# Kernel optimization log

Measured on AMD Instinct MI355X. Metric: run time of the kernel, lower is better.

The kernel has to match this reference:

```python
import jax, jax.numpy as jnp
import numpy as np

B, K, T, C = 4, 8, 2048, 64

def setup_inputs() -> dict:
    key = jax.random.key(0)
    ks = jax.random.split(key, 7)
    return {
        "x": jax.random.normal(ks[0], (B, K, T, C), dtype=jnp.float32),
        "Wq": jax.random.normal(ks[1], (C, C), dtype=jnp.float32) / np.sqrt(C),
        "bq": jax.random.normal(ks[2], (C,), dtype=jnp.float32) * 0.01,
        "Wk": jax.random.normal(ks[3], (C, C), dtype=jnp.float32) / np.sqrt(C),
        "bk": jax.random.normal(ks[4], (C,), dtype=jnp.float32) * 0.01,
        "Wv": jax.random.normal(ks[5], (C, C), dtype=jnp.float32) / np.sqrt(C),
        "bv": jax.random.normal(ks[6], (C,), dtype=jnp.float32) * 0.01,
    }

def reference(x, Wq, bq, Wk, bk, Wv, bv):
    c_dim = x.shape[-1]
    # torch nn.Linear: y = x @ W.T + b
    q = jnp.einsum('bktc,dc->bktd', x, Wq) + bq
    k = jnp.einsum('bktc,dc->bktd', x, Wk) + bk
    v = jnp.einsum('bktc,dc->bktd', x, Wv) + bv
    scores = jnp.einsum('bkic,bkjc->bkij', q, k) / jnp.sqrt(jnp.float32(c_dim))
    attn = jax.nn.softmax(scores, axis=-1)
    out = jnp.einsum('bkij,bkjc->bkic', attn, v)
    return out
```

## Files before the change

kernel.cpp:

```cpp
#include <hip/hip_runtime.h>


#define T_DIM 2048
#define NHEAD 32
#define HSTRIDE (T_DIM * 64)
#define QSCALE 0.18033688011112042f
#define SOFF  8.0f

#define SWZ(row, grp) ((row) * 64 + ((((grp) ^ ((row) & 7)) & 7) * 8))

typedef _Float16 h8 __attribute__((ext_vector_type(8)));
typedef _Float16 h4 __attribute__((ext_vector_type(4)));
typedef __fp16   g2 __attribute__((ext_vector_type(2)));
typedef float    f4 __attribute__((ext_vector_type(4)));

union H4U { h4 v; g2 p[2]; };
union H8U { h8 v; h4 h[2]; };

#if defined(__has_builtin)
#if __has_builtin(__builtin_amdgcn_exp2f)
#define EXP2(x) __builtin_amdgcn_exp2f(x)
#endif
#endif
#ifndef EXP2
__device__ inline float exp2_raw(float x) {
    float r;
    asm("v_exp_f32 %0, %1" : "=v"(r) : "v"(x));
    return r;
}
#define EXP2(x) exp2_raw(x)
#endif

__device__ inline h4 cvt4(f4 x) {
    H4U u;
    u.p[0] = __builtin_amdgcn_cvt_pkrtz(x[0], x[1]);
    u.p[1] = __builtin_amdgcn_cvt_pkrtz(x[2], x[3]);
    return u.v;
}

__global__ __launch_bounds__(256) void qkv_proj_kernel(
    const float* __restrict__ x,
    const float* __restrict__ Wq, const float* __restrict__ bq,
    const float* __restrict__ Wk, const float* __restrict__ bk,
    const float* __restrict__ Wv, const float* __restrict__ bv,
    _Float16* __restrict__ qh, _Float16* __restrict__ khT,
    _Float16* __restrict__ vtT)
{
    __shared__ _Float16 ws[3][64 * 64];
    __shared__ _Float16 xs[64 * 64];
    __shared__ float bsh[3][64];
    _Float16* ot = xs;

    const int tid  = threadIdx.x;
    const int row0 = blockIdx.x * 64;
    const int head = blockIdx.x >> 5;
    const int t0   = (blockIdx.x & 31) * 64;

    #pragma unroll
    for (int m = 0; m < 3; ++m) {
        const float* Wm = (m == 0) ? Wq : ((m == 1) ? Wk : Wv);
        const float* bm = (m == 0) ? bq : ((m == 1) ? bk : bv);
        #pragma unroll
        for (int pass = 0; pass < 4; ++pass) {
            const int idx = pass * 1024 + tid * 4;
            const int d = idx >> 6, c = idx & 63;
            f4 wv = *(const f4*)(Wm + idx);
            *(h4*)&ws[m][SWZ(d, c >> 3) + (c & 7)] = cvt4(wv);
        }
        if (tid < 64) bsh[m][tid] = bm[tid];
    }
    {
        const float* xb = x + (size_t)row0 * 64;
        #pragma unroll
        for (int pass = 0; pass < 4; ++pass) {
            const int idx = pass * 1024 + tid * 4;
            const int r = idx >> 6, c = idx & 63;
            f4 xv = *(const f4*)(xb + idx);
            *(h4*)&xs[SWZ(r, c >> 3) + (c & 7)] = cvt4(xv);
        }
    }
    __syncthreads();

    const int w    = tid >> 6;
    const int lane = tid & 63;
    const int l15  = lane & 15;
    const int qd   = lane >> 4;

    h8 af[2];
    #pragma unroll
    for (int ch = 0; ch < 2; ++ch)
        af[ch] = *(const h8*)&xs[SWZ(w * 16 + l15, ch * 4 + qd)];

    #pragma unroll
    for (int m = 0; m < 3; ++m) {
        h8 bf[4][2];
        #pragma unroll
        for (int ns = 0; ns < 4; ++ns)
            #pragma unroll
            for (int ch = 0; ch < 2; ++ch)
                bf[ns][ch] = *(const h8*)&ws[m][SWZ(ns * 16 + l15, ch * 4 + qd)];

        f4 acc[4];
        #pragma unroll
        for (int ns = 0; ns < 4; ++ns)
            acc[ns] = (f4){0.f, 0.f, 0.f, 0.f};
        #pragma unroll
        for (int ch = 0; ch < 2; ++ch)
            #pragma unroll
            for (int ns = 0; ns < 4; ++ns)
                acc[ns] = __builtin_amdgcn_mfma_f32_16x16x32_f16(
                    af[ch], bf[ns][ch], acc[ns], 0, 0, 0);

        __syncthreads();
        if (m < 2) {
            #pragma unroll
            for (int ns = 0; ns < 4; ++ns) {
                const int d = ns * 16 + l15;
                const float bias = bsh[m][d];
                #pragma unroll
                for (int r = 0; r < 4; ++r) {
                    const int t = w * 16 + qd * 4 + r;
                    float v = acc[ns][r] + bias;
                    if (m == 0) v *= QSCALE;
                    ot[SWZ(t, d >> 3) + (d & 7)] = (_Float16)v;
                }
            }
            __syncthreads();
            if (m == 0) {
                #pragma unroll
                for (int pass = 0; pass < 2; ++pass) {
                    const int t  = pass * 32 + (tid >> 3);
                    const int c0 = (tid & 7) * 8;
                    *(h8*)&qh[(size_t)(row0 + t) * 64 + c0] =
                        *(const h8*)&ot[SWZ(t, tid & 7)];
                }
            } else {
                #pragma unroll
                for (int pass = 0; pass < 2; ++pass) {
                    const int f    = pass * 2048 + tid * 8;
                    const int Jl   = f >> 10;
                    const int rest = f & 1023;
                    const int ch_  = rest >> 9;
                    const int qd_  = (rest >> 7) & 3;
                    const int l15_ = (rest >> 3) & 15;
                    h8 val = *(const h8*)&ot[SWZ(Jl * 16 + l15_, ch_ * 4 + qd_)];
                    *(h8*)&khT[(size_t)head * HSTRIDE + ((t0 >> 4) + Jl) * 1024 + rest] = val;
                }
            }
        } else {
            #pragma unroll
            for (int ns = 0; ns < 4; ++ns) {
                const int d = ns * 16 + l15;
                const float bias = bsh[2][d];
                const int tl = w * 16 + qd * 4;
                f4 pvf;
                #pragma unroll
                for (int r = 0; r < 4; ++r)
                    pvf[r] = acc[ns][r] + bias;
                *(h4*)&ot[SWZ(d, tl >> 3) + (tl & 7)] = cvt4(pvf);
            }
            __syncthreads();
            #pragma unroll
            for (int pass = 0; pass < 2; ++pass) {
                const int f   = pass * 2048 + tid * 8;
                const int qd3 = f >> 10;
                const int rem = f & 1023;
                const int c   = rem >> 4;
                const int g   = (rem & 15) >> 3;
                const int ta  = (2 * g) * 16 + qd3 * 4;
                const int tb  = ta + 16;
                H8U val;
                val.h[0] = *(const h4*)&ot[SWZ(c, ta >> 3) + (ta & 7)];
                val.h[1] = *(const h4*)&ot[SWZ(c, tb >> 3) + (tb & 7)];
                *(h8*)&vtT[(size_t)head * HSTRIDE + (t0 >> 6) * 4096 + f] = val.v;
            }
        }
    }
}

__global__ __launch_bounds__(256, 2) void attn_kernel(
    const _Float16* __restrict__ qh, const _Float16* __restrict__ khT,
    const _Float16* __restrict__ vtT, float* __restrict__ out)
{
    __shared__ float mrg[2][64][41];
    const int tid  = threadIdx.x;
    const int w    = tid >> 6;
    const int lane = tid & 63;
    const int l15  = lane & 15;
    const int qd   = lane >> 4;
    const int qgrp = w >> 1;
    const int kph  = w & 1;

    const int bid  = blockIdx.x;
    const int xcd  = bid & 7;
    const int slot = bid >> 3;
    const int head = xcd * 4 + (slot >> 5);
    const int q0   = (slot & 31) * 64 + qgrp * 32;

    h8 qf[2][2];
    #pragma unroll
    for (int is = 0; is < 2; ++is) {
        const _Float16* qp = qh + (size_t)(head * T_DIM + q0 + is * 16 + l15) * 64 + qd * 8;
        qf[is][0] = *(const h8*)qp;
        qf[is][1] = *(const h8*)(qp + 32);
    }

    const h4 vones = {(_Float16)1.0f, (_Float16)1.0f, (_Float16)1.0f, (_Float16)1.0f};
    f4 lacc[2] = {(f4){0.f,0.f,0.f,0.f}, (f4){0.f,0.f,0.f,0.f}};
    f4 oacc[2][4];
    #pragma unroll
    for (int is = 0; is < 2; ++is)
        #pragma unroll
        for (int cs = 0; cs < 4; ++cs)
            oacc[is][cs] = (f4){0.f, 0.f, 0.f, 0.f};

    const _Float16* kA = khT + (size_t)head * HSTRIDE + kph * 65536;
    const _Float16* kB = kA + 2048;
    const _Float16* vA = vtT + (size_t)head * HSTRIDE + kph * 65536;
    const int ko = lane * 8;
    const int vo = qd * 1024 + l15 * 16;

    h8 kf[4][2];
    #pragma unroll
    for (int jt = 0; jt < 4; ++jt)
        #pragma unroll
        for (int ch = 0; ch < 2; ++ch)
            kf[jt][ch] = *(const h8*)(((jt < 2) ? kA : kB) + (jt & 1) * 1024 + ch * 512 + ko);

    for (int kt = 0; kt < 16; ++kt) {
        H8U vf8[4][2];
        #pragma unroll
        for (int cs = 0; cs < 4; ++cs) {
            vf8[cs][0].v = *(const h8*)(vA + cs * 256 + vo);
            vf8[cs][1].v = *(const h8*)(vA + cs * 256 + vo + 8);
        }

        f4 st[4][2];
        #pragma unroll
        for (int jt = 0; jt < 4; ++jt)
            #pragma unroll
            for (int is = 0; is < 2; ++is)
                st[jt][is] = (f4){-SOFF, -SOFF, -SOFF, -SOFF};
        #pragma unroll
        for (int ch = 0; ch < 2; ++ch)
            #pragma unroll
            for (int jt = 0; jt < 4; ++jt)
                #pragma unroll
                for (int is = 0; is < 2; ++is)
                    st[jt][is] = __builtin_amdgcn_mfma_f32_16x16x32_f16(
                        kf[jt][ch], qf[is][ch], st[jt][is], 0, 0, 0);

        kA += 4096; kB += 4096;
        if (kt < 15) {
            #pragma unroll
            for (int jt = 0; jt < 4; ++jt)
                #pragma unroll
                for (int ch = 0; ch < 2; ++ch)
                    kf[jt][ch] = *(const h8*)(((jt < 2) ? kA : kB) + (jt & 1) * 1024 + ch * 512 + ko);
        }

        h4 pf[4][2];
        #pragma unroll
        for (int is = 0; is < 2; ++is)
            #pragma unroll
            for (int jt = 0; jt < 4; ++jt) {
                f4 p;
                p[0] = EXP2(st[jt][is][0]);
                p[1] = EXP2(st[jt][is][1]);
                p[2] = EXP2(st[jt][is][2]);
                p[3] = EXP2(st[jt][is][3]);
                pf[jt][is] = cvt4(p);
            }

        #pragma unroll
        for (int jt = 0; jt < 4; ++jt) {
            #pragma unroll
            for (int cs = 0; cs < 4; ++cs)
                #pragma unroll
                for (int is = 0; is < 2; ++is)
                    oacc[is][cs] = __builtin_amdgcn_mfma_f32_16x16x16f16(
                        pf[jt][is], vf8[cs][jt >> 1].h[jt & 1], oacc[is][cs], 0, 0, 0);
            #pragma unroll
            for (int is = 0; is < 2; ++is)
                lacc[is] = __builtin_amdgcn_mfma_f32_16x16x16f16(
                    pf[jt][is], vones, lacc[is], 0, 0, 0);
        }
        vA += 4096;
    }

    if (kph == 1) {
        #pragma unroll
        for (int is = 0; is < 2; ++is) {
            #pragma unroll
            for (int cs = 0; cs < 4; ++cs)
                #pragma unroll
                for (int r = 0; r < 4; ++r)
                    mrg[qgrp][lane][(is * 4 + cs) * 4 + r] = oacc[is][cs][r];
            #pragma unroll
            for (int r = 0; r < 4; ++r)
                mrg[qgrp][lane][32 + is * 4 + r] = lacc[is][r];
        }
    }
    __syncthreads();
    if (kph == 0) {
        #pragma unroll
        for (int is = 0; is < 2; ++is) {
            float linv[4];
            #pragma unroll
            for (int r = 0; r < 4; ++r)
                linv[r] = 1.f / (lacc[is][r] + mrg[qgrp][lane][32 + is * 4 + r]);
            #pragma unroll
            for (int cs = 0; cs < 4; ++cs) {
                const int c = cs * 16 + l15;
                #pragma unroll
                for (int r = 0; r < 4; ++r) {
                    const int t = q0 + is * 16 + qd * 4 + r;
                    float o = oacc[is][cs][r] + mrg[qgrp][lane][(is * 4 + cs) * 4 + r];
                    out[(size_t)(head * T_DIM + t) * 64 + c] = o * linv[r];
                }
            }
        }
    }
}

extern "C" void kernel_launch(void* const* d_in, const int* in_sizes, int n_in,
                              void* d_out, int out_size, void* d_ws, size_t ws_size,
                              hipStream_t stream)
{
    (void)in_sizes; (void)n_in; (void)out_size; (void)ws_size;
    const float* x  = (const float*)d_in[0];
    const float* Wq = (const float*)d_in[1];
    const float* bq = (const float*)d_in[2];
    const float* Wk = (const float*)d_in[3];
    const float* bk = (const float*)d_in[4];
    const float* Wv = (const float*)d_in[5];
    const float* bv = (const float*)d_in[6];
    float* out = (float*)d_out;

    _Float16* qh  = (_Float16*)d_ws;
    _Float16* khT = qh + (size_t)NHEAD * HSTRIDE;
    _Float16* vtT = khT + (size_t)NHEAD * HSTRIDE;

    hipLaunchKernelGGL(qkv_proj_kernel, dim3(1024), dim3(256), 0, stream,
                       x, Wq, bq, Wk, bk, Wv, bv, qh, khT, vtT);
    hipLaunchKernelGGL(attn_kernel, dim3(1024), dim3(256), 0, stream,
                       qh, khT, vtT, out);
}
```

Before: 131.0 us.

## Compute softmax row sums with VALU adds and shuffles instead of ones-MFMA

The attention kernel drops the extra MFMA against a ones matrix that accumulated the softmax denominators. It now adds the fp32 exp values per lane and reduces them across lanes with xor shuffles after the loop, then broadcasts the inverse with shuffles. The QKV projection also loads x straight from global memory into MFMA fragments, skipping the LDS staging buffer and one barrier. This trims matrix-core work in the inner loop and adds a few VALU adds and shuffles, and the row sum now uses unrounded fp32 probabilities.

Result: no change. 129.8 us (-0.9%).

```diff
diff --git a/kernel.cpp b/kernel.cpp
--- a/kernel.cpp
+++ b/kernel.cpp
@@ -38,6 +38,13 @@
     return u.v;
 }
 
+__device__ inline h8 cvt8(f4 a, f4 b) {
+    H8U r;
+    r.h[0] = cvt4(a);
+    r.h[1] = cvt4(b);
+    return r.v;
+}
+
 __global__ __launch_bounds__(256) void qkv_proj_kernel(
     const float* __restrict__ x,
     const float* __restrict__ Wq, const float* __restrict__ bq,
@@ -47,9 +54,8 @@
     _Float16* __restrict__ vtT)
 {
     __shared__ _Float16 ws[3][64 * 64];
-    __shared__ _Float16 xs[64 * 64];
+    __shared__ _Float16 ot[64 * 64];
     __shared__ float bsh[3][64];
-    _Float16* ot = xs;
 
     const int tid  = threadIdx.x;
     const int row0 = blockIdx.x * 64;
@@ -69,17 +75,6 @@
         }
         if (tid < 64) bsh[m][tid] = bm[tid];
     }
-    {
-        const float* xb = x + (size_t)row0 * 64;
-        #pragma unroll
-        for (int pass = 0; pass < 4; ++pass) {
-            const int idx = pass * 1024 + tid * 4;
-            const int r = idx >> 6, c = idx & 63;
-            f4 xv = *(const f4*)(xb + idx);
-            *(h4*)&xs[SWZ(r, c >> 3) + (c & 7)] = cvt4(xv);
-        }
-    }
-    __syncthreads();
 
     const int w    = tid >> 6;
     const int lane = tid & 63;
@@ -87,9 +82,16 @@
     const int qd   = lane >> 4;
 
     h8 af[2];
-    #pragma unroll
-    for (int ch = 0; ch < 2; ++ch)
-        af[ch] = *(const h8*)&xs[SWZ(w * 16 + l15, ch * 4 + qd)];
+    {
+        const float* xp = x + (size_t)(row0 + w * 16 + l15) * 64 + qd * 8;
+        #pragma unroll
+        for (int ch = 0; ch < 2; ++ch) {
+            f4 a0 = *(const f4*)(xp + ch * 32);
+            f4 a1 = *(const f4*)(xp + ch * 32 + 4);
+            af[ch] = cvt8(a0, a1);
+        }
+    }
+    __syncthreads();
 
     #pragma unroll
     for (int m = 0; m < 3; ++m) {
@@ -182,7 +184,7 @@
     const _Float16* __restrict__ qh, const _Float16* __restrict__ khT,
     const _Float16* __restrict__ vtT, float* __restrict__ out)
 {
-    __shared__ float mrg[2][64][41];
+    __shared__ float mrg[2][64][35];
     const int tid  = threadIdx.x;
     const int w    = tid >> 6;
     const int lane = tid & 63;
@@ -205,8 +207,7 @@
         qf[is][1] = *(const h8*)(qp + 32);
     }
 
-    const h4 vones = {(_Float16)1.0f, (_Float16)1.0f, (_Float16)1.0f, (_Float16)1.0f};
-    f4 lacc[2] = {(f4){0.f,0.f,0.f,0.f}, (f4){0.f,0.f,0.f,0.f}};
+    f4 rs4[2] = {(f4){0.f,0.f,0.f,0.f}, (f4){0.f,0.f,0.f,0.f}};
     f4 oacc[2][4];
     #pragma unroll
     for (int is = 0; is < 2; ++is)
@@ -269,23 +270,29 @@
                 p[1] = EXP2(st[jt][is][1]);
                 p[2] = EXP2(st[jt][is][2]);
                 p[3] = EXP2(st[jt][is][3]);
+                rs4[is] += p;
                 pf[jt][is] = cvt4(p);
             }
 
         #pragma unroll
-        for (int jt = 0; jt < 4; ++jt) {
+        for (int jt = 0; jt < 4; ++jt)
             #pragma unroll
             for (int cs = 0; cs < 4; ++cs)
                 #pragma unroll
                 for (int is = 0; is < 2; ++is)
                     oacc[is][cs] = __builtin_amdgcn_mfma_f32_16x16x16f16(
                         pf[jt][is], vf8[cs][jt >> 1].h[jt & 1], oacc[is][cs], 0, 0, 0);
-            #pragma unroll
-            for (int is = 0; is < 2; ++is)
-                lacc[is] = __builtin_amdgcn_mfma_f32_16x16x16f16(
-                    pf[jt][is], vones, lacc[is], 0, 0, 0);
-        }
+
         vA += 4096;
+    }
+
+    float lx[2];
+    #pragma unroll
+    for (int is = 0; is < 2; ++is) {
+        float l = (rs4[is][0] + rs4[is][1]) + (rs4[is][2] + rs4[is][3]);
+        l += __shfl_xor(l, 16, 64);
+        l += __shfl_xor(l, 32, 64);
+        lx[is] = l;
     }
 
     if (kph == 1) {
@@ -296,19 +303,18 @@
                 #pragma unroll
                 for (int r = 0; r < 4; ++r)
                     mrg[qgrp][lane][(is * 4 + cs) * 4 + r] = oacc[is][cs][r];
-            #pragma unroll
-            for (int r = 0; r < 4; ++r)
-                mrg[qgrp][lane][32 + is * 4 + r] = lacc[is][r];
+            mrg[qgrp][lane][32 + is] = lx[is];
         }
     }
     __syncthreads();
     if (kph == 0) {
         #pragma unroll
         for (int is = 0; is < 2; ++is) {
+            const float linvv = 1.f / (lx[is] + mrg[qgrp][lane][32 + is]);
             float linv[4];
             #pragma unroll
             for (int r = 0; r < 4; ++r)
-                linv[r] = 1.f / (lacc[is][r] + mrg[qgrp][lane][32 + is * 4 + r]);
+                linv[r] = __shfl(linvv, qd * 4 + r, 64);
             #pragma unroll
             for (int cs = 0; cs < 4; ++cs) {
                 const int c = cs * 16 + l15;
```
